# Optimization experiments

Hardware: AMD Instinct MI355X
Metric: run time of the kernel (lower is better)

Reference implementation:

```python
import jax, jax.numpy as jnp
import numpy as np

B, T, C, H, S = 4, 2048, 1024, 16, 64
LN_EPS = 1e-5
WKV_EPS = 1e-6
K_CLAMP = 30.0


def _ln(x, g, b):
    m = jnp.mean(x, axis=-1, keepdims=True)
    v = jnp.var(x, axis=-1, keepdims=True)
    return (x - m) * jax.lax.rsqrt(v + LN_EPS) * g + b


def _wkv(k, v, time_decay, time_first):
    # k, v: [B,T,H,S]; recurrence in fp32 over time
    decay = jnp.exp(-jnp.exp(time_decay.astype(jnp.float32)))  # [H,S]
    tf = jnp.exp(time_first.astype(jnp.float32))               # [H,S]
    kt = jnp.moveaxis(k, 1, 0).astype(jnp.float32)  # [T,B,H,S]
    vt = jnp.moveaxis(v, 1, 0).astype(jnp.float32)
    # t == 0 special case: state seeded with time_first factor
    w0 = jnp.exp(jnp.minimum(kt[0], K_CLAMP))
    num0 = tf * w0 * vt[0]
    den0 = tf * w0

    def step(carry, xs):
        num, den = carry
        kk, vv = xs
        w = jnp.exp(jnp.minimum(kk, K_CLAMP))
        num = decay * num + w * vv
        den = decay * den + w
        return (num, den), num / (den + WKV_EPS)

    (_, _), rest = jax.lax.scan(step, (num0, den0), (kt[1:], vt[1:]))
    out = jnp.concatenate([(num0 / (den0 + WKV_EPS))[None], rest], axis=0)  # [T,B,H,S]
    return jnp.moveaxis(out, 0, 1)  # [B,T,H,S]


def setup_inputs() -> dict:
    key = jax.random.key(0)
    ks = jax.random.split(key, 8)
    sc = 1.0 / np.sqrt(C)
    sc4 = 1.0 / np.sqrt(4 * C)
    return {
        "x": jax.random.normal(ks[0], (B, T, C), jnp.float32),
        "time_decay": jnp.full((H, S), -5.0, jnp.float32),
        "time_first": jnp.zeros((H, S), jnp.float32),
        "Wk": jax.random.normal(ks[1], (C, C), jnp.float32) * sc,
        "Wv": jax.random.normal(ks[2], (C, C), jnp.float32) * sc,
        "Wr": jax.random.normal(ks[3], (C, C), jnp.float32) * sc,
        "Wo": jax.random.normal(ks[4], (C, C), jnp.float32) * sc,
        "Wffk": jax.random.normal(ks[5], (4 * C, C), jnp.float32) * sc,
        "Wffv": jax.random.normal(ks[6], (C, 4 * C), jnp.float32) * sc4,
        "ln1_g": jnp.ones((C,), jnp.float32),
        "ln1_b": jnp.zeros((C,), jnp.float32),
        "ln2_g": jnp.ones((C,), jnp.float32),
        "ln2_b": jnp.zeros((C,), jnp.float32),
    }


def reference(x, time_decay, time_first, Wk, Wv, Wr, Wo, Wffk, Wffv, ln1_g, ln1_b, ln2_g, ln2_b):
    b, t, c = x.shape
    h, s = time_decay.shape
    xl = _ln(x, ln1_g, ln1_b)
    k = (xl @ Wk.T).reshape(b, t, h, s)
    v = (xl @ Wv.T).reshape(b, t, h, s)
    r = (xl @ Wr.T).reshape(b, t, h, s)
    wkv = _wkv(k, v, time_decay, time_first).astype(x.dtype)
    rwkv = (jax.nn.sigmoid(r) * wkv).reshape(b, t, c)
    x = x + rwkv @ Wo.T
    xl2 = _ln(x, ln2_g, ln2_b)
    ffn = (jax.nn.relu(xl2 @ Wffk.T) ** 2) @ Wffv.T
    return x + ffn
```

## Files before the change

### kernel.cpp

```cpp
#include <hip/hip_runtime.h>
#include <cstdint>
#include <cstddef>

#define TT 2048
#define CC 1024
#define HH 16
#define SS 64
#define MROWS 8192
#define KVRN 3072
#define NCH 32
#define LCH 64

using short8 = __attribute__((ext_vector_type(8))) short;
using f32x4  = __attribute__((ext_vector_type(4))) float;

__device__ __forceinline__ float b2f(unsigned short u) {
  union { unsigned int i; float f; } c; c.i = ((unsigned int)u) << 16; return c.f;
}
__device__ __forceinline__ unsigned short f2b(float f) {
  union { float f; unsigned int i; } c; c.f = f;
  unsigned int r = c.i + 0x7fffu + ((c.i >> 16) & 1u);
  return (unsigned short)(r >> 16);
}

typedef const __attribute__((address_space(1))) unsigned int* gas_ptr;
typedef __attribute__((address_space(3))) unsigned int* las_ptr;
__device__ __forceinline__ void gl_lds16(const unsigned short* g, unsigned short* l) {
  __builtin_amdgcn_global_load_lds((gas_ptr)g, (las_ptr)l, 16, 0, 0);
}

__global__ __launch_bounds__(256) void cvt_ln_kernel(const float* __restrict__ Wk,
                                                     const float* __restrict__ Wv,
                                                     const float* __restrict__ Wr,
                                                     const float* __restrict__ Wo,
                                                     const float* __restrict__ Wffk,
                                                     const float* __restrict__ Wffv,
                                                     unsigned short* __restrict__ dst,
                                                     const float* __restrict__ x,
                                                     const float* __restrict__ g,
                                                     const float* __restrict__ bta,
                                                     unsigned short* __restrict__ xlo) {
  const size_t M1 = 1048576;
  const int tid = threadIdx.x;
  if (blockIdx.x < 12288) {
    size_t i = ((size_t)blockIdx.x * 256 + tid) * 4;
    const float* src; size_t off;
    if      (i <  1 * M1) { src = Wk;   off = 0;      }
    else if (i <  2 * M1) { src = Wv;   off = 1 * M1; }
    else if (i <  3 * M1) { src = Wr;   off = 2 * M1; }
    else if (i <  4 * M1) { src = Wo;   off = 3 * M1; }
    else if (i <  8 * M1) { src = Wffk; off = 4 * M1; }
    else                  { src = Wffv; off = 8 * M1; }
    float4 v = *(const float4*)(src + (i - off));
    *(ushort4*)(dst + i) = make_ushort4(f2b(v.x), f2b(v.y), f2b(v.z), f2b(v.w));
    return;
  }
  const int row = blockIdx.x - 12288;
  const float* xr = x + (size_t)row * CC;
  float4 v = *(const float4*)(xr + tid * 4);
  float s  = v.x + v.y + v.z + v.w;
  float ss = v.x * v.x + v.y * v.y + v.z * v.z + v.w * v.w;
#pragma unroll
  for (int off = 32; off > 0; off >>= 1) {
    s  += __shfl_xor(s, off, 64);
    ss += __shfl_xor(ss, off, 64);
  }
  __shared__ float ls[4], lss[4];
  if ((tid & 63) == 0) { ls[tid >> 6] = s; lss[tid >> 6] = ss; }
  __syncthreads();
  s  = ls[0] + ls[1] + ls[2] + ls[3];
  ss = lss[0] + lss[1] + lss[2] + lss[3];
  const float mean = s * (1.0f / CC);
  const float var  = ss * (1.0f / CC) - mean * mean;
  const float rstd = rsqrtf(var + 1e-5f);
  float4 gv = *(const float4*)(g + tid * 4);
  float4 bv = *(const float4*)(bta + tid * 4);
  ushort4 o = make_ushort4(f2b((v.x - mean) * rstd * gv.x + bv.x),
                           f2b((v.y - mean) * rstd * gv.y + bv.y),
                           f2b((v.z - mean) * rstd * gv.z + bv.z),
                           f2b((v.w - mean) * rstd * gv.w + bv.w));
  *(ushort4*)(xlo + (size_t)row * CC + tid * 4) = o;
}

__global__ __launch_bounds__(256) void ln_kernel(const float* __restrict__ x,
                                                 const float* __restrict__ g,
                                                 const float* __restrict__ bta,
                                                 unsigned short* __restrict__ out) {
  const int row = blockIdx.x;
  const int tid = threadIdx.x;
  const float* xr = x + (size_t)row * CC;
  float4 v = *(const float4*)(xr + tid * 4);
  float s  = v.x + v.y + v.z + v.w;
  float ss = v.x * v.x + v.y * v.y + v.z * v.z + v.w * v.w;
#pragma unroll
  for (int off = 32; off > 0; off >>= 1) {
    s  += __shfl_xor(s, off, 64);
    ss += __shfl_xor(ss, off, 64);
  }
  __shared__ float ls[4], lss[4];
  if ((tid & 63) == 0) { ls[tid >> 6] = s; lss[tid >> 6] = ss; }
  __syncthreads();
  s  = ls[0] + ls[1] + ls[2] + ls[3];
  ss = lss[0] + lss[1] + lss[2] + lss[3];
  const float mean = s * (1.0f / CC);
  const float var  = ss * (1.0f / CC) - mean * mean;
  const float rstd = rsqrtf(var + 1e-5f);
  float4 gv = *(const float4*)(g + tid * 4);
  float4 bv = *(const float4*)(bta + tid * 4);
  ushort4 o = make_ushort4(f2b((v.x - mean) * rstd * gv.x + bv.x),
                           f2b((v.y - mean) * rstd * gv.y + bv.y),
                           f2b((v.z - mean) * rstd * gv.z + bv.z),
                           f2b((v.w - mean) * rstd * gv.w + bv.w));
  *(ushort4*)(out + (size_t)row * CC + tid * 4) = o;
}

__global__ __launch_bounds__(64) void wkv_local(const unsigned short* __restrict__ kvr,
                                                const float* __restrict__ td,
                                                const float* __restrict__ tfp,
                                                float* __restrict__ scratch) {
  const int blk = blockIdx.x;
  const int bh = blk >> 5, c = blk & (NCH - 1);
  const int b = bh >> 4, h = bh & 15;
  const int s = threadIdx.x;
  const int ch = h * SS + s;
  const float e = __expf(td[ch]);
  const float d = __expf(-e);
  const float tfir = __expf(tfp[ch]);
  size_t idx = ((size_t)b * TT + (size_t)c * LCH) * KVRN + ch;
  float num = 0.f, den = 0.f;
  for (int i = 0; i < LCH; ++i) {
    float w = __expf(fminf(b2f(kvr[idx]), 30.f));
    if (c == 0 && i == 0) w *= tfir;
    float vv = b2f(kvr[idx + 1024]);
    num = d * num + w * vv;
    den = d * den + w;
    idx += KVRN;
  }
  float* o = scratch + ((size_t)bh * NCH + c) * 128;
  o[s] = num; o[64 + s] = den;
}

__global__ __launch_bounds__(64) void wkv_emit(const unsigned short* __restrict__ kvr,
                                               const float* __restrict__ td,
                                               const float* __restrict__ tfp,
                                               const float* __restrict__ scratch,
                                               unsigned short* __restrict__ rwkv) {
  const int blk = blockIdx.x;
  const int bh = blk >> 5, c = blk & (NCH - 1);
  const int b = bh >> 4, h = bh & 15;
  const int s = threadIdx.x;
  const int ch = h * SS + s;
  const float e = __expf(td[ch]);
  const float d = __expf(-e);
  const float Dc = __expf(-e * (float)LCH);
  const float tfir = __expf(tfp[ch]);
  float num = 0.f, den = 0.f;
  const float* sc = scratch + (size_t)bh * NCH * 128;
  for (int cc = 0; cc < c; ++cc) {
    num = Dc * num + sc[cc * 128 + s];
    den = Dc * den + sc[cc * 128 + 64 + s];
  }
  size_t idx = ((size_t)b * TT + (size_t)c * LCH) * KVRN + ch;
  size_t odx = ((size_t)b * TT + (size_t)c * LCH) * CC + ch;
  for (int i = 0; i < LCH; ++i) {
    float w = __expf(fminf(b2f(kvr[idx]), 30.f));
    if (c == 0 && i == 0) w *= tfir;
    float vv = b2f(kvr[idx + 1024]);
    num = d * num + w * vv;
    den = d * den + w;
    float o = num / (den + 1e-6f);
    float rr = b2f(kvr[idx + 2048]);
    float sg = 1.0f / (1.0f + __expf(-rr));
    rwkv[odx] = f2b(sg * o);
    idx += KVRN;
    odx += CC;
  }
}

template <int EP>
__global__ __launch_bounds__(256, 3) void gemm_bt(const unsigned short* __restrict__ A,
                                                  const unsigned short* __restrict__ Bw,
                                                  void* __restrict__ outv,
                                                  const float* __restrict__ res,
                                                  int N, int K) {
  __shared__ __align__(16) unsigned short As[3][128 * 32];
  __shared__ __align__(16) unsigned short Bs[3][128 * 32];
  const int tid = threadIdx.x;

  const int nbn = N >> 7;
  const int per_grp = nbn << 4;
  const int bid = blockIdx.x;
  const int grp = bid / per_grp;
  const int rem = bid - grp * per_grp;
  const int bm = (grp << 4) + (rem & 15);
  const int bn = rem >> 4;

  const int ch0 = tid, ch1 = tid + 256;
  const int r0 = ch0 >> 2, q0 = (ch0 & 3) ^ ((ch0 >> 3) & 3);
  const int r1 = ch1 >> 2, q1 = (ch1 & 3) ^ ((ch1 >> 3) & 3);
  const unsigned short* ga0 = A  + (size_t)(bm * 128 + r0) * K + q0 * 8;
  const unsigned short* ga1 = A  + (size_t)(bm * 128 + r1) * K + q1 * 8;
  const unsigned short* gb0 = Bw + (size_t)(bn * 128 + r0) * K + q0 * 8;
  const unsigned short* gb1 = Bw + (size_t)(bn * 128 + r1) * K + q1 * 8;
  const int so0 = ch0 * 8, so1 = ch1 * 8;

  const int lane = tid & 63;
  const int w    = tid >> 6;
  const int q    = lane >> 4, r16 = lane & 15;
  const int qs   = q ^ ((r16 >> 1) & 3);
  const int wrow = (w >> 1) * 64, wcol = (w & 1) * 64;

  f32x4 acc[4][4] = {};

  auto stage = [&](int b3) {
    gl_lds16(ga0, &As[b3][so0]);
    gl_lds16(ga1, &As[b3][so1]);
    gl_lds16(gb0, &Bs[b3][so0]);
    gl_lds16(gb1, &Bs[b3][so1]);
    ga0 += 32; ga1 += 32; gb0 += 32; gb1 += 32;
  };

  const int iters = K >> 5;
  stage(0);
  stage(1);

  int cb = 0, pb = 2;
  for (int i = 0; i < iters; ++i) {
    __builtin_amdgcn_s_waitcnt(0x0F74);
    __builtin_amdgcn_sched_barrier(0);
    asm volatile("s_barrier");
    __builtin_amdgcn_sched_barrier(0);
    if (i + 2 < iters) stage(pb);

    const unsigned short* Ab = &As[cb][0];
    const unsigned short* Bb = &Bs[cb][0];
    short8 af[4], bfr[4];
#pragma unroll
    for (int mi = 0; mi < 4; ++mi)
      af[mi] = *(const short8*)(Ab + ((wrow + mi * 16 + r16) * 4 + qs) * 8);
#pragma unroll
    for (int ni = 0; ni < 4; ++ni)
      bfr[ni] = *(const short8*)(Bb + ((wcol + ni * 16 + r16) * 4 + qs) * 8);
#pragma unroll
    for (int mi = 0; mi < 4; ++mi)
#pragma unroll
      for (int ni = 0; ni < 4; ++ni)
        acc[mi][ni] = __builtin_amdgcn_mfma_f32_16x16x32_bf16(af[mi], bfr[ni], acc[mi][ni], 0, 0, 0);

    cb = (cb == 2) ? 0 : cb + 1;
    pb = (pb == 2) ? 0 : pb + 1;
  }

#pragma unroll
  for (int mi = 0; mi < 4; ++mi) {
#pragma unroll
    for (int r = 0; r < 4; ++r) {
      const int grow = bm * 128 + wrow + mi * 16 + q * 4 + r;
#pragma unroll
      for (int ni = 0; ni < 4; ++ni) {
        const int gcol = bn * 128 + wcol + ni * 16 + r16;
        const size_t idx = (size_t)grow * N + gcol;
        float vv = acc[mi][ni][r];
        if (EP == 2) {
          ((float*)outv)[idx] = res[idx] + vv;
        } else {
          if (EP == 1) { vv = fmaxf(vv, 0.0f); vv = vv * vv; }
          ((unsigned short*)outv)[idx] = f2b(vv);
        }
      }
    }
  }
}

extern "C" void kernel_launch(void* const* d_in, const int* in_sizes, int n_in,
                              void* d_out, int out_size, void* d_ws, size_t ws_size,
                              hipStream_t stream) {
  const float* x    = (const float*)d_in[0];
  const float* td   = (const float*)d_in[1];
  const float* tf   = (const float*)d_in[2];
  const float* Wk   = (const float*)d_in[3];
  const float* Wv   = (const float*)d_in[4];
  const float* Wr   = (const float*)d_in[5];
  const float* Wo   = (const float*)d_in[6];
  const float* Wffk = (const float*)d_in[7];
  const float* Wffv = (const float*)d_in[8];
  const float* g1   = (const float*)d_in[9];
  const float* b1   = (const float*)d_in[10];
  const float* g2   = (const float*)d_in[11];
  const float* b2   = (const float*)d_in[12];
  float* out = (float*)d_out;

  char* ws = (char*)d_ws;
  const size_t MB = 1024ull * 1024ull;
  unsigned short* WB    = (unsigned short*)ws;
  unsigned short* WkvrB = WB;
  unsigned short* WoB   = WB + 3 * 1048576;
  unsigned short* WfkB  = WB + 4 * 1048576;
  unsigned short* WfvB  = WB + 8 * 1048576;
  unsigned short* xl    = (unsigned short*)(ws + 24 * MB);
  unsigned short* kvr   = (unsigned short*)(ws + 40 * MB);
  float*          x2    = (float*)(ws + 88 * MB);
  unsigned short* hb    = (unsigned short*)(ws + 120 * MB);
  float*          wkvS  = (float*)(ws + 184 * MB);
  unsigned short* rwkv  = xl;
  unsigned short* xl2   = kvr;

  cvt_ln_kernel<<<12288 + MROWS, 256, 0, stream>>>(Wk, Wv, Wr, Wo, Wffk, Wffv, WB,
                                                   x, g1, b1, xl);

  gemm_bt<0><<<(KVRN / 128) * (MROWS / 128), 256, 0, stream>>>(xl, WkvrB, kvr, nullptr, KVRN, 1024);

  wkv_local<<<64 * NCH, 64, 0, stream>>>(kvr, td, tf, wkvS);
  wkv_emit<<<64 * NCH, 64, 0, stream>>>(kvr, td, tf, wkvS, rwkv);

  gemm_bt<2><<<(CC / 128) * (MROWS / 128), 256, 0, stream>>>(rwkv, WoB, x2, x, 1024, 1024);

  ln_kernel<<<MROWS, 256, 0, stream>>>(x2, g2, b2, xl2);

  gemm_bt<1><<<(4096 / 128) * (MROWS / 128), 256, 0, stream>>>(xl2, WfkB, hb, nullptr, 4096, 1024);

  gemm_bt<2><<<(CC / 128) * (MROWS / 128), 256, 0, stream>>>(hb, WfvB, out, x2, 1024, 4096);
}
```

Before: 438.6 us.

## Switch GEMMs to 256x256 tiles with 512 threads and split-K atomic FFN-down

Replaces the 128x128, 256-thread GEMM with a 256x256 tile kernel using 8 waves. It double-buffers LDS in two K-halves, interleaves global-to-LDS staging with MFMA phases, and raises wave priority during MFMA. The final FFN-down GEMM is split-K by 2 and accumulates into the output with float atomics. The output is pre-seeded with the residual x2 by the second layernorm kernel. The larger tiles aim to improve data reuse and MFMA density. In exchange, the 128-block grids give poor occupancy for N=1024, and atomics add contention and nondeterministic summation order.

Result: slower. 485.2 us (+10.6%).

```diff
diff --git a/kernel.cpp b/kernel.cpp
--- a/kernel.cpp
+++ b/kernel.cpp
@@ -85,11 +85,13 @@
 __global__ __launch_bounds__(256) void ln_kernel(const float* __restrict__ x,
                                                  const float* __restrict__ g,
                                                  const float* __restrict__ bta,
-                                                 unsigned short* __restrict__ out) {
+                                                 unsigned short* __restrict__ out,
+                                                 float* __restrict__ outc) {
   const int row = blockIdx.x;
   const int tid = threadIdx.x;
   const float* xr = x + (size_t)row * CC;
   float4 v = *(const float4*)(xr + tid * 4);
+  *(float4*)(outc + (size_t)row * CC + tid * 4) = v;
   float s  = v.x + v.y + v.z + v.w;
   float ss = v.x * v.x + v.y * v.y + v.z * v.z + v.w * v.w;
 #pragma unroll
@@ -177,92 +179,157 @@
   }
 }
 
+#define GBAR do { __builtin_amdgcn_sched_barrier(0); __builtin_amdgcn_s_barrier(); \
+                  __builtin_amdgcn_sched_barrier(0); } while (0)
+#define WAIT_LGKM0 do { __builtin_amdgcn_s_waitcnt(0xC07F); \
+                        __builtin_amdgcn_sched_barrier(0); } while (0)
+#define WAIT_VM8   do { __builtin_amdgcn_sched_barrier(0); \
+                        __builtin_amdgcn_s_waitcnt(0x0F78); \
+                        __builtin_amdgcn_sched_barrier(0); } while (0)
+
 template <int EP>
-__global__ __launch_bounds__(256, 3) void gemm_bt(const unsigned short* __restrict__ A,
+__global__ __launch_bounds__(512, 2) void gemm256(const unsigned short* __restrict__ A,
                                                   const unsigned short* __restrict__ Bw,
                                                   void* __restrict__ outv,
                                                   const float* __restrict__ res,
-                                                  int N, int K) {
-  __shared__ __align__(16) unsigned short As[3][128 * 32];
-  __shared__ __align__(16) unsigned short Bs[3][128 * 32];
+                                                  int N, int Kfull, int Kloop) {
+  __shared__ __align__(16) unsigned short As[2][2][256][32];
+  __shared__ __align__(16) unsigned short Bs[2][2][256][32];
   const int tid = threadIdx.x;
 
-  const int nbn = N >> 7;
+  const int nbn = N >> 8;
   const int per_grp = nbn << 4;
   const int bid = blockIdx.x;
   const int grp = bid / per_grp;
   const int rem = bid - grp * per_grp;
   const int bm = (grp << 4) + (rem & 15);
   const int bn = rem >> 4;
-
-  const int ch0 = tid, ch1 = tid + 256;
-  const int r0 = ch0 >> 2, q0 = (ch0 & 3) ^ ((ch0 >> 3) & 3);
-  const int r1 = ch1 >> 2, q1 = (ch1 & 3) ^ ((ch1 >> 3) & 3);
-  const unsigned short* ga0 = A  + (size_t)(bm * 128 + r0) * K + q0 * 8;
-  const unsigned short* ga1 = A  + (size_t)(bm * 128 + r1) * K + q1 * 8;
-  const unsigned short* gb0 = Bw + (size_t)(bn * 128 + r0) * K + q0 * 8;
-  const unsigned short* gb1 = Bw + (size_t)(bn * 128 + r1) * K + q1 * 8;
-  const int so0 = ch0 * 8, so1 = ch1 * 8;
-
-  const int lane = tid & 63;
-  const int w    = tid >> 6;
-  const int q    = lane >> 4, r16 = lane & 15;
-  const int qs   = q ^ ((r16 >> 1) & 3);
-  const int wrow = (w >> 1) * 64, wcol = (w & 1) * 64;
-
-  f32x4 acc[4][4] = {};
-
-  auto stage = [&](int b3) {
-    gl_lds16(ga0, &As[b3][so0]);
-    gl_lds16(ga1, &As[b3][so1]);
-    gl_lds16(gb0, &Bs[b3][so0]);
-    gl_lds16(gb1, &Bs[b3][so1]);
-    ga0 += 32; ga1 += 32; gb0 += 32; gb1 += 32;
+  const int koffb = blockIdx.y * Kloop;
+  const int nt = Kloop >> 6;
+
+  const int r0  = tid >> 2;
+  const int qsl = ((tid & 3) ^ (r0 & 3)) << 3;
+  const unsigned short* gA0 = A  + (size_t)(bm * 256 + r0) * Kfull + koffb + qsl;
+  const unsigned short* gA1 = gA0 + (size_t)128 * Kfull;
+  const unsigned short* gB0 = Bw + (size_t)(bn * 256 + r0) * Kfull + koffb + qsl;
+  const unsigned short* gB1 = gB0 + (size_t)128 * Kfull;
+  const int ldsoff = tid * 8;
+
+  auto stA = [&](int bb, int kk, int ko) {
+    unsigned short* d = &As[bb][kk][0][0];
+    gl_lds16(gA0 + ko, d + ldsoff);
+    gl_lds16(gA1 + ko, d + ldsoff + 4096);
   };
-
-  const int iters = K >> 5;
-  stage(0);
-  stage(1);
-
-  int cb = 0, pb = 2;
-  for (int i = 0; i < iters; ++i) {
-    __builtin_amdgcn_s_waitcnt(0x0F74);
-    __builtin_amdgcn_sched_barrier(0);
-    asm volatile("s_barrier");
-    __builtin_amdgcn_sched_barrier(0);
-    if (i + 2 < iters) stage(pb);
-
-    const unsigned short* Ab = &As[cb][0];
-    const unsigned short* Bb = &Bs[cb][0];
-    short8 af[4], bfr[4];
+  auto stB = [&](int bb, int kk, int ko) {
+    unsigned short* d = &Bs[bb][kk][0][0];
+    gl_lds16(gB0 + ko, d + ldsoff);
+    gl_lds16(gB1 + ko, d + ldsoff + 4096);
+  };
+
+  const int lane = tid & 63, w = tid >> 6;
+  const int wr = w >> 2, wn = w & 3;
+  const int r16 = lane & 15, q = lane >> 4;
+  const int qx = (q ^ (r16 & 3)) << 3;
+  const unsigned short* fA = &As[0][0][0][0] + (wr * 128 + r16) * 32 + qx;
+  const unsigned short* fB = &Bs[0][0][0][0] + (wn * 64  + r16) * 32 + qx;
+
+  f32x4 acc[8][4] = {};
+  short8 af[4], bf_[4];
+
+  stA(0, 0, 0);  stB(0, 0, 0);
+  stA(0, 1, 32); stB(0, 1, 32);
+  stA(1, 0, 64); stB(1, 0, 64);
+  WAIT_VM8;
+  GBAR;
+
+  int b = 0;
+  for (int t = 0; t < nt; ++t, b ^= 1) {
+    const unsigned short* fAb = fA + b * 16384;
+    const unsigned short* fBb = fB + b * 16384;
+    const int t1 = (t + 1 < nt) ? t + 1 : nt - 1;
+    const int t2 = (t + 2 < nt) ? t + 2 : nt - 1;
+    const int ko1 = (t1 << 6) + 32;
+    const int ko2 = (t2 << 6);
+
+#pragma unroll
+    for (int i = 0; i < 4; ++i) af[i]  = *(const short8*)(fAb + i * 512);
+#pragma unroll
+    for (int i = 0; i < 4; ++i) bf_[i] = *(const short8*)(fBb + i * 512);
+    stA(b ^ 1, 1, ko1);
+    GBAR;
+    WAIT_LGKM0;
+    __builtin_amdgcn_s_setprio(1);
 #pragma unroll
     for (int mi = 0; mi < 4; ++mi)
-      af[mi] = *(const short8*)(Ab + ((wrow + mi * 16 + r16) * 4 + qs) * 8);
-#pragma unroll
-    for (int ni = 0; ni < 4; ++ni)
-      bfr[ni] = *(const short8*)(Bb + ((wcol + ni * 16 + r16) * 4 + qs) * 8);
+#pragma unroll
+      for (int ni = 0; ni < 4; ++ni)
+        acc[mi][ni] = __builtin_amdgcn_mfma_f32_16x16x32_bf16(af[mi], bf_[ni], acc[mi][ni], 0, 0, 0);
+    __builtin_amdgcn_s_setprio(0);
+    GBAR;
+
+#pragma unroll
+    for (int i = 0; i < 4; ++i) af[i] = *(const short8*)(fAb + (4 + i) * 512);
+    stB(b ^ 1, 1, ko1);
+    WAIT_VM8;
+    GBAR;
+    WAIT_LGKM0;
+    __builtin_amdgcn_s_setprio(1);
 #pragma unroll
     for (int mi = 0; mi < 4; ++mi)
 #pragma unroll
       for (int ni = 0; ni < 4; ++ni)
-        acc[mi][ni] = __builtin_amdgcn_mfma_f32_16x16x32_bf16(af[mi], bfr[ni], acc[mi][ni], 0, 0, 0);
-
-    cb = (cb == 2) ? 0 : cb + 1;
-    pb = (pb == 2) ? 0 : pb + 1;
-  }
-
-#pragma unroll
-  for (int mi = 0; mi < 4; ++mi) {
+        acc[4 + mi][ni] = __builtin_amdgcn_mfma_f32_16x16x32_bf16(af[mi], bf_[ni], acc[4 + mi][ni], 0, 0, 0);
+    __builtin_amdgcn_s_setprio(0);
+    GBAR;
+
+#pragma unroll
+    for (int i = 0; i < 4; ++i) af[i]  = *(const short8*)(fAb + 8192 + i * 512);
+#pragma unroll
+    for (int i = 0; i < 4; ++i) bf_[i] = *(const short8*)(fBb + 8192 + i * 512);
+    stA(b, 0, ko2);
+    GBAR;
+    WAIT_LGKM0;
+    __builtin_amdgcn_s_setprio(1);
+#pragma unroll
+    for (int mi = 0; mi < 4; ++mi)
+#pragma unroll
+      for (int ni = 0; ni < 4; ++ni)
+        acc[mi][ni] = __builtin_amdgcn_mfma_f32_16x16x32_bf16(af[mi], bf_[ni], acc[mi][ni], 0, 0, 0);
+    __builtin_amdgcn_s_setprio(0);
+    GBAR;
+
+#pragma unroll
+    for (int i = 0; i < 4; ++i) af[i] = *(const short8*)(fAb + 8192 + (4 + i) * 512);
+    stB(b, 0, ko2);
+    WAIT_VM8;
+    GBAR;
+    WAIT_LGKM0;
+    __builtin_amdgcn_s_setprio(1);
+#pragma unroll
+    for (int mi = 0; mi < 4; ++mi)
+#pragma unroll
+      for (int ni = 0; ni < 4; ++ni)
+        acc[4 + mi][ni] = __builtin_amdgcn_mfma_f32_16x16x32_bf16(af[mi], bf_[ni], acc[4 + mi][ni], 0, 0, 0);
+    __builtin_amdgcn_s_setprio(0);
+    GBAR;
+  }
+
+  __builtin_amdgcn_s_waitcnt(0x0070);
+
+#pragma unroll
+  for (int mi = 0; mi < 8; ++mi) {
 #pragma unroll
     for (int r = 0; r < 4; ++r) {
-      const int grow = bm * 128 + wrow + mi * 16 + q * 4 + r;
+      const int grow = bm * 256 + wr * 128 + mi * 16 + q * 4 + r;
 #pragma unroll
       for (int ni = 0; ni < 4; ++ni) {
-        const int gcol = bn * 128 + wcol + ni * 16 + r16;
+        const int gcol = bn * 256 + wn * 64 + ni * 16 + r16;
         const size_t idx = (size_t)grow * N + gcol;
         float vv = acc[mi][ni][r];
         if (EP == 2) {
           ((float*)outv)[idx] = res[idx] + vv;
+        } else if (EP == 3) {
+          unsafeAtomicAdd((float*)outv + idx, vv);
         } else {
           if (EP == 1) { vv = fmaxf(vv, 0.0f); vv = vv * vv; }
           ((unsigned short*)outv)[idx] = f2b(vv);
@@ -308,16 +375,20 @@
   cvt_ln_kernel<<<12288 + MROWS, 256, 0, stream>>>(Wk, Wv, Wr, Wo, Wffk, Wffv, WB,
                                                    x, g1, b1, xl);
 
-  gemm_bt<0><<<(KVRN / 128) * (MROWS / 128), 256, 0, stream>>>(xl, WkvrB, kvr, nullptr, KVRN, 1024);
+  gemm256<0><<<dim3((KVRN / 256) * (MROWS / 256), 1), 512, 0, stream>>>(
+      xl, WkvrB, kvr, nullptr, KVRN, 1024, 1024);
 
   wkv_local<<<64 * NCH, 64, 0, stream>>>(kvr, td, tf, wkvS);
   wkv_emit<<<64 * NCH, 64, 0, stream>>>(kvr, td, tf, wkvS, rwkv);
 
-  gemm_bt<2><<<(CC / 128) * (MROWS / 128), 256, 0, stream>>>(rwkv, WoB, x2, x, 1024, 1024);
-
-  ln_kernel<<<MROWS, 256, 0, stream>>>(x2, g2, b2, xl2);
-
-  gemm_bt<1><<<(4096 / 128) * (MROWS / 128), 256, 0, stream>>>(xl2, WfkB, hb, nullptr, 4096, 1024);
-
-  gemm_bt<2><<<(CC / 128) * (MROWS / 128), 256, 0, stream>>>(hb, WfvB, out, x2, 1024, 4096);
-}
+  gemm256<2><<<dim3((CC / 256) * (MROWS / 256), 1), 512, 0, stream>>>(
+      rwkv, WoB, x2, x, CC, 1024, 1024);
+
+  ln_kernel<<<MROWS, 256, 0, stream>>>(x2, g2, b2, xl2, out);
+
+  gemm256<1><<<dim3((4096 / 256) * (MROWS / 256), 1), 512, 0, stream>>>(
+      xl2, WfkB, hb, nullptr, 4096, 1024, 1024);
+
+  gemm256<3><<<dim3((CC / 256) * (MROWS / 256), 2), 512, 0, stream>>>(
+      hb, WfvB, out, nullptr, CC, 4096, 2048);
+}
```

## Use 256x128 GEMM tiles with split-K atomic residual accumulation

Applied to the files above, without the earlier changes.

Adds a wider GEMM kernel with 256x128 tiles, triple-buffered LDS staging and a grouped block order, and uses it for the output projection and both FFN matmuls. The output projection and the FFN down-projection split K across two blocks and atomically add into a buffer that already holds the residual. The LayerNorm kernels now copy their input rows into that buffer so the residual seeds the atomic sum. The aim is more reuse per tile and enough blocks to fill the GPU on the N=1024 GEMMs. In exchange it adds extra residual copy traffic, atomic-add contention, and summation order that is no longer deterministic.

Result: slower. 503.4 us (+14.8%).

```diff
diff --git a/kernel.cpp b/kernel.cpp
--- a/kernel.cpp
+++ b/kernel.cpp
@@ -39,7 +39,8 @@
                                                      const float* __restrict__ x,
                                                      const float* __restrict__ g,
                                                      const float* __restrict__ bta,
-                                                     unsigned short* __restrict__ xlo) {
+                                                     unsigned short* __restrict__ xlo,
+                                                     float* __restrict__ x2o) {
   const size_t M1 = 1048576;
   const int tid = threadIdx.x;
   if (blockIdx.x < 12288) {
@@ -58,6 +59,7 @@
   const int row = blockIdx.x - 12288;
   const float* xr = x + (size_t)row * CC;
   float4 v = *(const float4*)(xr + tid * 4);
+  *(float4*)(x2o + (size_t)row * CC + tid * 4) = v;
   float s  = v.x + v.y + v.z + v.w;
   float ss = v.x * v.x + v.y * v.y + v.z * v.z + v.w * v.w;
 #pragma unroll
@@ -85,11 +87,13 @@
 __global__ __launch_bounds__(256) void ln_kernel(const float* __restrict__ x,
                                                  const float* __restrict__ g,
                                                  const float* __restrict__ bta,
-                                                 unsigned short* __restrict__ out) {
+                                                 unsigned short* __restrict__ out,
+                                                 float* __restrict__ outc) {
   const int row = blockIdx.x;
   const int tid = threadIdx.x;
   const float* xr = x + (size_t)row * CC;
   float4 v = *(const float4*)(xr + tid * 4);
+  *(float4*)(outc + (size_t)row * CC + tid * 4) = v;
   float s  = v.x + v.y + v.z + v.w;
   float ss = v.x * v.x + v.y * v.y + v.z * v.z + v.w * v.w;
 #pragma unroll
@@ -272,6 +276,105 @@
   }
 }
 
+template <int EP>
+__global__ __launch_bounds__(256, 2) void gemm_wide(const unsigned short* __restrict__ A,
+                                                    const unsigned short* __restrict__ Bw,
+                                                    void* __restrict__ outv,
+                                                    int N, int Kfull, int Kloop) {
+  __shared__ __align__(16) unsigned short As[3][256 * 32];
+  __shared__ __align__(16) unsigned short Bs[3][128 * 32];
+  const int tid = threadIdx.x;
+
+  const int nbn = N >> 7;
+  const int per_grp = nbn << 4;
+  const int bid = blockIdx.x;
+  const int grp = bid / per_grp;
+  const int rem = bid - grp * per_grp;
+  const int bm = (grp << 4) + (rem & 15);
+  const int bn = rem >> 4;
+  const int koffb = blockIdx.y * Kloop;
+  const int iters = Kloop >> 5;
+
+  const int r0  = tid >> 2;
+  const int qsl = ((tid & 3) ^ ((tid >> 3) & 3)) << 3;
+  const unsigned short* gA[4];
+  const unsigned short* gB[2];
+#pragma unroll
+  for (int m = 0; m < 4; ++m)
+    gA[m] = A + (size_t)(bm * 256 + r0 + 64 * m) * Kfull + koffb + qsl;
+#pragma unroll
+  for (int m = 0; m < 2; ++m)
+    gB[m] = Bw + (size_t)(bn * 128 + r0 + 64 * m) * Kfull + koffb + qsl;
+  const int so = tid * 8;
+
+  auto stage = [&](int b3) {
+    unsigned short* da = &As[b3][0];
+    unsigned short* db = &Bs[b3][0];
+#pragma unroll
+    for (int m = 0; m < 4; ++m) { gl_lds16(gA[m], da + so + 2048 * m); gA[m] += 32; }
+#pragma unroll
+    for (int m = 0; m < 2; ++m) { gl_lds16(gB[m], db + so + 2048 * m); gB[m] += 32; }
+  };
+
+  const int lane = tid & 63;
+  const int w    = tid >> 6;
+  const int q    = lane >> 4, r16 = lane & 15;
+  const int qs   = q ^ ((r16 >> 1) & 3);
+  const int wrow = (w >> 1) * 128, wcol = (w & 1) * 64;
+
+  f32x4 acc[8][4] = {};
+
+  stage(0);
+  stage(1);
+
+  int cb = 0, pb = 2;
+  for (int i = 0; i < iters; ++i) {
+    __builtin_amdgcn_s_waitcnt(0x0F76);
+    __builtin_amdgcn_sched_barrier(0);
+    asm volatile("s_barrier");
+    __builtin_amdgcn_sched_barrier(0);
+    if (i + 2 < iters) stage(pb);
+
+    const unsigned short* Ab = &As[cb][0];
+    const unsigned short* Bb = &Bs[cb][0];
+    short8 af[8], bfr[4];
+#pragma unroll
+    for (int mi = 0; mi < 8; ++mi)
+      af[mi] = *(const short8*)(Ab + ((wrow + mi * 16 + r16) * 4 + qs) * 8);
+#pragma unroll
+    for (int ni = 0; ni < 4; ++ni)
+      bfr[ni] = *(const short8*)(Bb + ((wcol + ni * 16 + r16) * 4 + qs) * 8);
+#pragma unroll
+    for (int mi = 0; mi < 8; ++mi)
+#pragma unroll
+      for (int ni = 0; ni < 4; ++ni)
+        acc[mi][ni] = __builtin_amdgcn_mfma_f32_16x16x32_bf16(af[mi], bfr[ni], acc[mi][ni], 0, 0, 0);
+
+    cb = (cb == 2) ? 0 : cb + 1;
+    pb = (pb == 2) ? 0 : pb + 1;
+  }
+
+#pragma unroll
+  for (int mi = 0; mi < 8; ++mi) {
+#pragma unroll
+    for (int r = 0; r < 4; ++r) {
+      const int grow = bm * 256 + wrow + mi * 16 + q * 4 + r;
+#pragma unroll
+      for (int ni = 0; ni < 4; ++ni) {
+        const int gcol = bn * 128 + wcol + ni * 16 + r16;
+        const size_t idx = (size_t)grow * N + gcol;
+        float vv = acc[mi][ni][r];
+        if (EP == 3) {
+          unsafeAtomicAdd((float*)outv + idx, vv);
+        } else {
+          if (EP == 1) { vv = fmaxf(vv, 0.0f); vv = vv * vv; }
+          ((unsigned short*)outv)[idx] = f2b(vv);
+        }
+      }
+    }
+  }
+}
+
 extern "C" void kernel_launch(void* const* d_in, const int* in_sizes, int n_in,
                               void* d_out, int out_size, void* d_ws, size_t ws_size,
                               hipStream_t stream) {
@@ -306,18 +409,21 @@
   unsigned short* xl2   = kvr;
 
   cvt_ln_kernel<<<12288 + MROWS, 256, 0, stream>>>(Wk, Wv, Wr, Wo, Wffk, Wffv, WB,
-                                                   x, g1, b1, xl);
+                                                   x, g1, b1, xl, x2);
 
   gemm_bt<0><<<(KVRN / 128) * (MROWS / 128), 256, 0, stream>>>(xl, WkvrB, kvr, nullptr, KVRN, 1024);
 
   wkv_local<<<64 * NCH, 64, 0, stream>>>(kvr, td, tf, wkvS);
   wkv_emit<<<64 * NCH, 64, 0, stream>>>(kvr, td, tf, wkvS, rwkv);
 
-  gemm_bt<2><<<(CC / 128) * (MROWS / 128), 256, 0, stream>>>(rwkv, WoB, x2, x, 1024, 1024);
-
-  ln_kernel<<<MROWS, 256, 0, stream>>>(x2, g2, b2, xl2);
-
-  gemm_bt<1><<<(4096 / 128) * (MROWS / 128), 256, 0, stream>>>(xl2, WfkB, hb, nullptr, 4096, 1024);
-
-  gemm_bt<2><<<(CC / 128) * (MROWS / 128), 256, 0, stream>>>(hb, WfvB, out, x2, 1024, 4096);
-}
+  gemm_wide<3><<<dim3((MROWS / 256) * (CC / 128), 2), 256, 0, stream>>>(
+      rwkv, WoB, x2, CC, 1024, 512);
+
+  ln_kernel<<<MROWS, 256, 0, stream>>>(x2, g2, b2, xl2, out);
+
+  gemm_wide<1><<<dim3((MROWS / 256) * (4096 / 128), 1), 256, 0, stream>>>(
+      xl2, WfkB, hb, 4096, 1024, 1024);
+
+  gemm_wide<3><<<dim3((MROWS / 256) * (CC / 128), 2), 256, 0, stream>>>(
+      hb, WfvB, out, CC, 4096, 2048);
+}
```

## Split-K the N=1024 GEMMs with atomic accumulation into residual-seeded outputs

Applied to the files above, without the earlier changes.

The two output-projection GEMMs with N=1024 (Wo and Wffv) now run as split-K with two K halves on blockIdx.y, and each half atomically adds into an fp32 output. That output is pre-seeded with the residual by the preceding LN kernels, which now also copy their input row out. The goal is to double the block count for these GEMMs, which launched only 512 tiles, and so fill more of the device's CUs. In exchange it adds an extra full-tensor fp32 write in each LN kernel and atomic read-modify-write traffic, and the fp32 summation order is no longer deterministic.

New measurement: 533.2 us. +21.6%, slower.

```diff
diff --git a/kernel.cpp b/kernel.cpp
--- a/kernel.cpp
+++ b/kernel.cpp
@@ -39,7 +39,8 @@
                                                      const float* __restrict__ x,
                                                      const float* __restrict__ g,
                                                      const float* __restrict__ bta,
-                                                     unsigned short* __restrict__ xlo) {
+                                                     unsigned short* __restrict__ xlo,
+                                                     float* __restrict__ x2o) {
   const size_t M1 = 1048576;
   const int tid = threadIdx.x;
   if (blockIdx.x < 12288) {
@@ -58,6 +59,7 @@
   const int row = blockIdx.x - 12288;
   const float* xr = x + (size_t)row * CC;
   float4 v = *(const float4*)(xr + tid * 4);
+  *(float4*)(x2o + (size_t)row * CC + tid * 4) = v;
   float s  = v.x + v.y + v.z + v.w;
   float ss = v.x * v.x + v.y * v.y + v.z * v.z + v.w * v.w;
 #pragma unroll
@@ -85,11 +87,13 @@
 __global__ __launch_bounds__(256) void ln_kernel(const float* __restrict__ x,
                                                  const float* __restrict__ g,
                                                  const float* __restrict__ bta,
-                                                 unsigned short* __restrict__ out) {
+                                                 unsigned short* __restrict__ out,
+                                                 float* __restrict__ outc) {
   const int row = blockIdx.x;
   const int tid = threadIdx.x;
   const float* xr = x + (size_t)row * CC;
   float4 v = *(const float4*)(xr + tid * 4);
+  *(float4*)(outc + (size_t)row * CC + tid * 4) = v;
   float s  = v.x + v.y + v.z + v.w;
   float ss = v.x * v.x + v.y * v.y + v.z * v.z + v.w * v.w;
 #pragma unroll
@@ -182,7 +186,7 @@
                                                   const unsigned short* __restrict__ Bw,
                                                   void* __restrict__ outv,
                                                   const float* __restrict__ res,
-                                                  int N, int K) {
+                                                  int N, int Kfull, int Kloop) {
   __shared__ __align__(16) unsigned short As[3][128 * 32];
   __shared__ __align__(16) unsigned short Bs[3][128 * 32];
   const int tid = threadIdx.x;
@@ -194,14 +198,15 @@
   const int rem = bid - grp * per_grp;
   const int bm = (grp << 4) + (rem & 15);
   const int bn = rem >> 4;
+  const int koff = blockIdx.y * Kloop;
 
   const int ch0 = tid, ch1 = tid + 256;
   const int r0 = ch0 >> 2, q0 = (ch0 & 3) ^ ((ch0 >> 3) & 3);
   const int r1 = ch1 >> 2, q1 = (ch1 & 3) ^ ((ch1 >> 3) & 3);
-  const unsigned short* ga0 = A  + (size_t)(bm * 128 + r0) * K + q0 * 8;
-  const unsigned short* ga1 = A  + (size_t)(bm * 128 + r1) * K + q1 * 8;
-  const unsigned short* gb0 = Bw + (size_t)(bn * 128 + r0) * K + q0 * 8;
-  const unsigned short* gb1 = Bw + (size_t)(bn * 128 + r1) * K + q1 * 8;
+  const unsigned short* ga0 = A  + (size_t)(bm * 128 + r0) * Kfull + koff + q0 * 8;
+  const unsigned short* ga1 = A  + (size_t)(bm * 128 + r1) * Kfull + koff + q1 * 8;
+  const unsigned short* gb0 = Bw + (size_t)(bn * 128 + r0) * Kfull + koff + q0 * 8;
+  const unsigned short* gb1 = Bw + (size_t)(bn * 128 + r1) * Kfull + koff + q1 * 8;
   const int so0 = ch0 * 8, so1 = ch1 * 8;
 
   const int lane = tid & 63;
@@ -220,7 +225,7 @@
     ga0 += 32; ga1 += 32; gb0 += 32; gb1 += 32;
   };
 
-  const int iters = K >> 5;
+  const int iters = Kloop >> 5;
   stage(0);
   stage(1);
 
@@ -263,6 +268,8 @@
         float vv = acc[mi][ni][r];
         if (EP == 2) {
           ((float*)outv)[idx] = res[idx] + vv;
+        } else if (EP == 3) {
+          unsafeAtomicAdd((float*)outv + idx, vv);
         } else {
           if (EP == 1) { vv = fmaxf(vv, 0.0f); vv = vv * vv; }
           ((unsigned short*)outv)[idx] = f2b(vv);
@@ -306,18 +313,22 @@
   unsigned short* xl2   = kvr;
 
   cvt_ln_kernel<<<12288 + MROWS, 256, 0, stream>>>(Wk, Wv, Wr, Wo, Wffk, Wffv, WB,
-                                                   x, g1, b1, xl);
-
-  gemm_bt<0><<<(KVRN / 128) * (MROWS / 128), 256, 0, stream>>>(xl, WkvrB, kvr, nullptr, KVRN, 1024);
+                                                   x, g1, b1, xl, x2);
+
+  gemm_bt<0><<<(KVRN / 128) * (MROWS / 128), 256, 0, stream>>>(
+      xl, WkvrB, kvr, nullptr, KVRN, 1024, 1024);
 
   wkv_local<<<64 * NCH, 64, 0, stream>>>(kvr, td, tf, wkvS);
   wkv_emit<<<64 * NCH, 64, 0, stream>>>(kvr, td, tf, wkvS, rwkv);
 
-  gemm_bt<2><<<(CC / 128) * (MROWS / 128), 256, 0, stream>>>(rwkv, WoB, x2, x, 1024, 1024);
-
-  ln_kernel<<<MROWS, 256, 0, stream>>>(x2, g2, b2, xl2);
-
-  gemm_bt<1><<<(4096 / 128) * (MROWS / 128), 256, 0, stream>>>(xl2, WfkB, hb, nullptr, 4096, 1024);
-
-  gemm_bt<2><<<(CC / 128) * (MROWS / 128), 256, 0, stream>>>(hb, WfvB, out, x2, 1024, 4096);
-}
+  gemm_bt<3><<<dim3((CC / 128) * (MROWS / 128), 2), 256, 0, stream>>>(
+      rwkv, WoB, x2, nullptr, CC, 1024, 512);
+
+  ln_kernel<<<MROWS, 256, 0, stream>>>(x2, g2, b2, xl2, out);
+
+  gemm_bt<1><<<(4096 / 128) * (MROWS / 128), 256, 0, stream>>>(
+      xl2, WfkB, hb, nullptr, 4096, 1024, 1024);
+
+  gemm_bt<3><<<dim3((CC / 128) * (MROWS / 128), 2), 256, 0, stream>>>(
+      hb, WfvB, out, nullptr, CC, 4096, 2048);
+}
```
